# Kernel optimization log

Measured on AMD Instinct MI355X. Metric: run time of the kernel, lower is better.

The kernel has to match this reference:

```python
import jax, jax.numpy as jnp
import numpy as np

N = 100000          # n_nodes
E = 1600000         # n_edges (avg degree 16)
IN = 256            # in_dim
OUT = 16            # out_dim
SLOPE = 0.2         # leaky_relu negative slope
DROP = 0.5          # dropout rate


def _xavier(key, shape):
    fan_in, fan_out = shape
    std = (2.0 / (fan_in + fan_out)) ** 0.5
    return std * jax.random.normal(key, shape, jnp.float32)


def setup_inputs() -> dict:
    key = jax.random.key(0)
    ks = jax.random.split(key, 10)
    x = jax.random.normal(ks[0], (N, IN), jnp.float32)
    row = jax.random.randint(ks[1], (E,), 0, N, jnp.int32)
    col = jax.random.randint(ks[2], (E,), 0, N, jnp.int32)
    edge_w = jax.random.uniform(ks[3], (E,), jnp.float32)
    W1 = _xavier(ks[4], (IN, IN // 2)); b1 = jnp.zeros((IN // 2,), jnp.float32)
    W2 = _xavier(ks[5], (IN // 2, IN // 4)); b2 = jnp.zeros((IN // 4,), jnp.float32)
    W3 = _xavier(ks[6], (IN // 4, IN // 8)); b3 = jnp.zeros((IN // 8,), jnp.float32)
    W4 = _xavier(ks[7], (IN // 8, OUT)); b4 = jnp.zeros((OUT,), jnp.float32)
    # dropout mask (training-mode dropout made deterministic; pre-scaled by 1/(1-p))
    drop_mask = (jax.random.uniform(ks[8], (N, IN // 2)) > DROP).astype(jnp.float32) / (1.0 - DROP)
    return dict(x=x, row=row, col=col, edge_w=edge_w,
                W1=W1, b1=b1, W2=W2, b2=b2, W3=W3, b3=b3, W4=W4, b4=b4,
                drop_mask=drop_mask)


def reference(x, row, col, edge_w, W1, b1, W2, b2, W3, b3, W4, b4, drop_mask):
    def spmm(h):
        # out[i] = sum over edges (i <- j): w_ij * h[j]   (sparse adj @ h)
        return jax.ops.segment_sum(edge_w[:, None] * h[col], row, num_segments=N)

    lrelu = lambda v: jax.nn.leaky_relu(v, SLOPE)

    h = spmm(x @ W1) + b1          # gc1: [N, IN/2]
    h = lrelu(h) * drop_mask       # leaky_relu + dropout
    h = spmm(h @ W2) + b2          # gc2: [N, IN/4]
    h = lrelu(h)
    h = lrelu(h @ W3 + b3)         # clf hidden: [N, IN/8]
    return h @ W4 + b4             # logits: [N, OUT]
```

## Files before the change

kernel.cpp:

```cpp
#include <hip/hip_runtime.h>
#include <hip/hip_bf16.h>

#define N_NODES 100000
#define N_EDGES 1600000
#define SLOPE_ 0.2f
#define NBK 196
#define NGRP 8
#define BCAPG 1280
#define BCAP 9216
#define NCB 13
#define KEYS (512 * NCB)
#define BINBLK 256
#define PREPW 20
#define PMBLK 1563

typedef __attribute__((ext_vector_type(8))) short bf16x8;
typedef __attribute__((ext_vector_type(4))) float f32x4;

__device__ __forceinline__ short f2bf(float f) {
    __hip_bfloat16 h = __float2bfloat16(f);
    return *reinterpret_cast<short*>(&h);
}
__device__ __forceinline__ float bflo(unsigned u) { return __uint_as_float(u << 16); }
__device__ __forceinline__ float bfhi(unsigned u) { return __uint_as_float(u & 0xFFFF0000u); }
__device__ __forceinline__ float bf2f(short s) {
    return __uint_as_float(((unsigned)(unsigned short)s) << 16);
}


__global__ void zero_k(int* __restrict__ cur8) {
    for (int i = threadIdx.x; i < NBK * NGRP; i += 256) cur8[i] = 0;
}


__global__ void passA_k(const int* __restrict__ row, const int* __restrict__ col,
                        const float* __restrict__ ew, int* __restrict__ cur8,
                        int2* __restrict__ binned,
                        const float* __restrict__ W1, const float* __restrict__ W2,
                        const float* __restrict__ mask,
                        short* __restrict__ Bp1, short* __restrict__ Bp2,
                        unsigned* __restrict__ mp) {
    int t = threadIdx.x;
    if (blockIdx.x < BINBLK) {
        __shared__ int hist[NBK], base[NBK], off[NBK];
        int g = blockIdx.x & (NGRP - 1);
        const int chunk = N_EDGES / BINBLK;
        int e0 = blockIdx.x * chunk;
        for (int i = t; i < NBK; i += 256) { hist[i] = 0; off[i] = 0; }
        __syncthreads();
        for (int i = t; i < chunk; i += 256)
            atomicAdd(&hist[row[e0 + i] >> 9], 1);
        __syncthreads();
        for (int i = t; i < NBK; i += 256)
            base[i] = atomicAdd(&cur8[i * NGRP + g], hist[i]);
        __syncthreads();
        for (int i = t; i < chunk; i += 256) {
            int e = e0 + i;
            int r = row[e], c = col[e];
            int b = r >> 9;
            int p = base[b] + atomicAdd(&off[b], 1);
            if (p < BCAPG)
                binned[((size_t)(b * NGRP + g)) * BCAPG + p] =
                    make_int2(((r & 511) << 17) | c, __float_as_int(ew[e]));
        }
        return;
    }
    int bi = blockIdx.x - BINBLK;
    if (bi < PREPW) {
        int i = bi * 256 + t;
        if (i < 4096) {
            int ln = i & 15, nt = (i >> 4) & 7, g = (i >> 7) & 3, ks = i >> 9;
            int n = nt * 16 + ln, k0 = ks * 32 + g * 8;
            bf16x8 v;
#pragma unroll
            for (int j = 0; j < 8; j++) v[j] = f2bf(W1[(k0 + j) * 128 + n]);
            *(bf16x8*)(Bp1 + (size_t)i * 8) = v;
        } else if (i < 5120) {
            int c = i - 4096;
            int ln = c & 15, nt = (c >> 4) & 3, g = (c >> 6) & 3, ks = c >> 8;
            int n = nt * 16 + ln, k0 = ks * 32 + g * 8;
            bf16x8 v;
#pragma unroll
            for (int j = 0; j < 8; j++) v[j] = f2bf(W2[(k0 + j) * 64 + n]);
            *(bf16x8*)(Bp2 + (size_t)c * 8) = v;
        }
        return;
    }
    int pb = bi - PREPW;
    long fbase = (long)pb * 8192;
    int wv = t >> 6, lane = t & 63;
    const long FLIM = (long)N_NODES * 128;
    for (int it = 0; it < 32; ++it) {
        long f = fbase + it * 256 + wv * 64 + lane;
        float v = (f < FLIM) ? mask[f] : 0.f;
        unsigned long long bl = __ballot(v != 0.f);
        if (lane == 0) {
            long w = f >> 5;
            if (w < (long)N_NODES * 4)
                *(unsigned long long*)(mp + w) = bl;
        }
    }
}


__global__ void __launch_bounds__(512) passB_k(const int2* __restrict__ binned,
                                               const int* __restrict__ cur8,
                                               unsigned* __restrict__ cw,
                                               int* __restrict__ row_ptr) {
    __shared__ int hist[KEYS];
    __shared__ int offs[KEYS];
    __shared__ int ssum[512];
    __shared__ int bexc[256];
    int t = threadIdx.x, b = blockIdx.x;

    int cnt_g[NGRP];
    int cnt = 0;
#pragma unroll
    for (int g = 0; g < NGRP; g++) {
        cnt_g[g] = min(cur8[b * NGRP + g], BCAPG);
        cnt += cnt_g[g];
    }
    if (cnt > BCAP) cnt = BCAP;

    if (t < 256) {
        int tot = 0;
        if (t < NBK) {
#pragma unroll
            for (int g = 0; g < NGRP; g++) tot += min(cur8[t * NGRP + g], BCAPG);
            if (tot > BCAP) tot = BCAP;
        }
        bexc[t] = tot;
    }
    __syncthreads();
    for (int off2 = 1; off2 < 256; off2 <<= 1) {
        int v = (t < 256 && t >= off2) ? bexc[t - off2] : 0;
        __syncthreads();
        if (t < 256) bexc[t] += v;
        __syncthreads();
    }
    int gbase = bexc[b] - cnt;

    for (int i = t; i < KEYS; i += 512) hist[i] = 0;
    __syncthreads();

#pragma unroll
    for (int g = 0; g < NGRP; g++) {
        const int2* src = binned + ((size_t)(b * NGRP + g)) * BCAPG;
        int cg = cnt_g[g];
        for (int i = t; i < cg; i += 512) {
            int2 v = src[i];
            int c = v.x & 0x1FFFF, lr = v.x >> 17;
            atomicAdd(&hist[lr * NCB + (c >> 13)], 1);
        }
    }
    __syncthreads();

    int loc[NCB];
    int tot = 0;
#pragma unroll
    for (int j = 0; j < NCB; j++) {
        loc[j] = tot;
        tot += hist[t * NCB + j];
    }
    ssum[t] = tot;
    __syncthreads();
    for (int off2 = 1; off2 < 512; off2 <<= 1) {
        int v = (t >= off2) ? ssum[t - off2] : 0;
        __syncthreads();
        ssum[t] += v;
        __syncthreads();
    }
    int base = ssum[t] - tot;
#pragma unroll
    for (int j = 0; j < NCB; j++) offs[t * NCB + j] = base + loc[j];

    int grow = b * 512 + t;
    if (grow <= N_NODES) row_ptr[grow] = gbase + base;
    __syncthreads();

#pragma unroll
    for (int g = 0; g < NGRP; g++) {
        const int2* src = binned + ((size_t)(b * NGRP + g)) * BCAPG;
        int cg = cnt_g[g];
        for (int i = t; i < cg; i += 512) {
            int2 v = src[i];
            int c = v.x & 0x1FFFF, lr = v.x >> 17;
            int p = gbase + atomicAdd(&offs[lr * NCB + (c >> 13)], 1);
            unsigned wb = (unsigned)(unsigned short)f2bf(__int_as_float(v.y));
            cw[p] = ((unsigned)c << 15) | (wb & 0x7FFFu);
        }
    }
}


template <int K, int COLS, bool ABF16>
__global__ __launch_bounds__(512) void gemm_p(const void* __restrict__ Ap,
                                              const short* __restrict__ Bp,
                                              short* __restrict__ out, int M) {
    constexpr int NT = COLS / 16;
    constexpr int NKS = K / 32;
    __shared__ short Bs[K * COLS];
    int t = threadIdx.x;
    for (int i = t; i < K * COLS / 8; i += 512)
        *(bf16x8*)(Bs + (size_t)i * 8) = *(const bf16x8*)(Bp + (size_t)i * 8);
    __syncthreads();

    int l = t & 63, wv = t >> 6;
    int ln = l & 15, g = l >> 4;
    int row0 = blockIdx.x * 256 + wv * 32;
    int r0 = row0 + ln, r1 = row0 + 16 + ln;
    int cr0 = min(r0, M - 1), cr1 = min(r1, M - 1);

    f32x4 acc[2][NT];
#pragma unroll
    for (int rf = 0; rf < 2; rf++)
#pragma unroll
        for (int nt = 0; nt < NT; nt++) acc[rf][nt] = (f32x4){0.f, 0.f, 0.f, 0.f};

#pragma unroll
    for (int ks = 0; ks < NKS; ks++) {
        int kk = ks * 32 + g * 8;
        bf16x8 a0, a1;
        if constexpr (ABF16) {
            a0 = *(const bf16x8*)((const short*)Ap + (size_t)cr0 * K + kk);
            a1 = *(const bf16x8*)((const short*)Ap + (size_t)cr1 * K + kk);
        } else {
            const float* p0 = (const float*)Ap + (size_t)cr0 * K + kk;
            const float* p1 = (const float*)Ap + (size_t)cr1 * K + kk;
            float4 u0 = *(const float4*)p0;
            float4 u1 = *(const float4*)(p0 + 4);
            float4 v0 = *(const float4*)p1;
            float4 v1 = *(const float4*)(p1 + 4);
            a0[0] = f2bf(u0.x); a0[1] = f2bf(u0.y); a0[2] = f2bf(u0.z); a0[3] = f2bf(u0.w);
            a0[4] = f2bf(u1.x); a0[5] = f2bf(u1.y); a0[6] = f2bf(u1.z); a0[7] = f2bf(u1.w);
            a1[0] = f2bf(v0.x); a1[1] = f2bf(v0.y); a1[2] = f2bf(v0.z); a1[3] = f2bf(v0.w);
            a1[4] = f2bf(v1.x); a1[5] = f2bf(v1.y); a1[6] = f2bf(v1.z); a1[7] = f2bf(v1.w);
        }
#pragma unroll
        for (int nt = 0; nt < NT; nt++) {
            bf16x8 b = *(const bf16x8*)(Bs + (size_t)((((ks * 4 + g) * NT + nt) * 16 + ln)) * 8);
            acc[0][nt] = __builtin_amdgcn_mfma_f32_16x16x32_bf16(a0, b, acc[0][nt], 0, 0, 0);
            acc[1][nt] = __builtin_amdgcn_mfma_f32_16x16x32_bf16(a1, b, acc[1][nt], 0, 0, 0);
        }
    }
#pragma unroll
    for (int rf = 0; rf < 2; rf++)
#pragma unroll
        for (int nt = 0; nt < NT; nt++)
#pragma unroll
            for (int r = 0; r < 4; r++) {
                int orow = row0 + rf * 16 + g * 4 + r;
                if (orow < M) out[(size_t)orow * COLS + nt * 16 + ln] = f2bf(acc[rf][nt][r]);
            }
}


template <int D, bool DROP>
__global__ void spmm_bf(const int* __restrict__ row_ptr, const unsigned* __restrict__ cwp,
                        const short* __restrict__ h,
                        const float* __restrict__ bias, const unsigned* __restrict__ maskp,
                        short* __restrict__ out, int n) {
    int bid = blockIdx.x;
    int sbid = (bid & 7) * 3125 + (bid >> 3);
    int wid = sbid * 4 + (int)(threadIdx.x >> 6);
    int lane = threadIdx.x & 63;
    if (wid >= n) return;
    int sp = __builtin_amdgcn_readfirstlane(row_ptr[wid]);
    int ep = __builtin_amdgcn_readfirstlane(row_ptr[wid + 1]);
    int cnt = ep - sp;
    const unsigned* pcw = cwp + sp;
    const unsigned* hb = (const unsigned*)h;
    float ax = 0.f, ay = 0.f;

    if (D == 128) {
        for (int jb = 0; jb < cnt; jb += 8) {
            unsigned u[8];
            float w[8];
#pragma unroll
            for (int p = 0; p < 8; p++) {
                int idx = jb + p;
                unsigned md = pcw[idx];
                md = (idx < cnt) ? md : 0u;
                int c = (int)(md >> 15);
                w[p] = __uint_as_float((md & 0x7FFFu) << 16);
                u[p] = hb[(size_t)c * 64 + lane];
            }
#pragma unroll
            for (int p = 0; p < 8; p++) {
                ax += w[p] * bflo(u[p]);
                ay += w[p] * bfhi(u[p]);
            }
        }
        float2 b = *(const float2*)(bias + 2 * lane);
        float ox = ax + b.x, oy = ay + b.y;
        ox = ox > 0.f ? ox : SLOPE_ * ox;
        oy = oy > 0.f ? oy : SLOPE_ * oy;
        if (DROP) {
            unsigned mw = maskp[(size_t)wid * 4 + (lane >> 4)];
            unsigned sh = (2 * lane) & 31;
            ox = ((mw >> sh) & 1u) ? 2.f * ox : 0.f;
            oy = ((mw >> (sh + 1)) & 1u) ? 2.f * oy : 0.f;
        }
        unsigned ov = (unsigned)(unsigned short)f2bf(ox) |
                      ((unsigned)(unsigned short)f2bf(oy) << 16);
        *(unsigned*)(out + (size_t)wid * 128 + 2 * lane) = ov;
    } else {
        int li = lane & 31;
        for (int jb = 0; jb < cnt; jb += 8) {
            unsigned u[4];
            float w[4];
#pragma unroll
            for (int p = 0; p < 4; p++) {
                int iA = jb + 2 * p, iB = iA + 1;
                unsigned mA = pcw[iA];
                mA = (iA < cnt) ? mA : 0u;
                unsigned mB = pcw[iB];
                mB = (iB < cnt) ? mB : 0u;
                unsigned md = (lane < 32) ? mA : mB;
                int c = (int)(md >> 15);
                w[p] = __uint_as_float((md & 0x7FFFu) << 16);
                u[p] = hb[(size_t)c * 32 + li];
            }
#pragma unroll
            for (int p = 0; p < 4; p++) {
                ax += w[p] * bflo(u[p]);
                ay += w[p] * bfhi(u[p]);
            }
        }
        ax += __shfl_xor(ax, 32);
        ay += __shfl_xor(ay, 32);
        float2 b = *(const float2*)(bias + li * 2);
        float ox = ax + b.x, oy = ay + b.y;
        ox = ox > 0.f ? ox : SLOPE_ * ox;
        oy = oy > 0.f ? oy : SLOPE_ * oy;
        unsigned ov = (unsigned)(unsigned short)f2bf(ox) |
                      ((unsigned)(unsigned short)f2bf(oy) << 16);
        if (lane < 32) *(unsigned*)(out + (size_t)wid * 64 + li * 2) = ov;
    }
}


__global__ void clf_k(const short* __restrict__ h, const float* __restrict__ W3,
                      const float* __restrict__ b3, const float* __restrict__ W4,
                      const float* __restrict__ b4, float* __restrict__ out) {
    __shared__ float W3s[64][32];
    __shared__ float W4s[32][16];
    __shared__ float b3s[32], b4s[16];
    __shared__ float hs[32][64];
    __shared__ float t4[32][33];
    int t = threadIdx.x;
    for (int l = t; l < 64 * 32; l += 256) W3s[l / 32][l % 32] = W3[l];
    for (int l = t; l < 32 * 16; l += 256) W4s[l / 16][l % 16] = W4[l];
    if (t < 32) b3s[t] = b3[t];
    if (t < 16) b4s[t] = b4[t];
    int row0 = blockIdx.x * 32;
    {
        bf16x8 v = *(const bf16x8*)(h + (size_t)row0 * 64 + t * 8);
        int r = t >> 3, c0 = (t & 7) << 3;
#pragma unroll
        for (int j = 0; j < 8; j++) hs[r][c0 + j] = bf2f(v[j]);
    }
    __syncthreads();
    for (int l = t; l < 1024; l += 256) {
        int r = l / 32, c = l % 32;
        float a = b3s[c];
#pragma unroll 8
        for (int k = 0; k < 64; k++) a += hs[r][k] * W3s[k][c];
        t4[r][c] = a > 0.f ? a : SLOPE_ * a;
    }
    __syncthreads();
    for (int l = t; l < 512; l += 256) {
        int r = l / 16, c = l % 16;
        float a = b4s[c];
#pragma unroll
        for (int k = 0; k < 32; k++) a += t4[r][k] * W4s[k][c];
        out[(size_t)(row0 + r) * 16 + c] = a;
    }
}


extern "C" void kernel_launch(void* const* d_in, const int* in_sizes, int n_in,
                              void* d_out, int out_size, void* d_ws, size_t ws_size,
                              hipStream_t stream) {
    const float* x = (const float*)d_in[0];
    const int* row = (const int*)d_in[1];
    const int* col = (const int*)d_in[2];
    const float* ew = (const float*)d_in[3];
    const float* W1 = (const float*)d_in[4];
    const float* b1 = (const float*)d_in[5];
    const float* W2 = (const float*)d_in[6];
    const float* b2 = (const float*)d_in[7];
    const float* W3 = (const float*)d_in[8];
    const float* b3 = (const float*)d_in[9];
    const float* W4 = (const float*)d_in[10];
    const float* b4 = (const float*)d_in[11];
    const float* mask = (const float*)d_in[12];
    float* out = (float*)d_out;

    const int N = N_NODES, E = N_EDGES;

    short* h0 = (short*)d_ws;
    short* h1 = h0 + (size_t)N * 128;
    short* h2 = h1 + (size_t)N * 128;
    short* h3 = h2 + (size_t)N * 64;
    short* Bp1 = h3 + (size_t)N * 64;
    short* Bp2 = Bp1 + 32768;
    int* row_ptr = (int*)(Bp2 + 8192);
    int* cur8 = row_ptr + N + 1;
    unsigned* mask_p = (unsigned*)(cur8 + NBK * NGRP + 8);
    unsigned* cwp = mask_p + (size_t)N * 4;
    int2* binned = (int2*)h0;

    zero_k<<<1, 256, 0, stream>>>(cur8);
    passA_k<<<BINBLK + PREPW + PMBLK, 256, 0, stream>>>(row, col, ew, cur8, binned,
                                                        W1, W2, mask, Bp1, Bp2, mask_p);
    passB_k<<<NBK, 512, 0, stream>>>(binned, cur8, cwp, row_ptr);

    gemm_p<256, 128, false><<<(N + 255) / 256, 512, 0, stream>>>(x, Bp1, h0, N);
    spmm_bf<128, true><<<25000, 256, 0, stream>>>(row_ptr, cwp, h0, b1, mask_p, h1, N);
    gemm_p<128, 64, true><<<(N + 255) / 256, 512, 0, stream>>>(h1, Bp2, h2, N);
    spmm_bf<64, false><<<25000, 256, 0, stream>>>(row_ptr, cwp, h2, b2, nullptr, h3, N);
    clf_k<<<N / 32, 256, 0, stream>>>(h3, W3, b3, W4, b4, out);
}
```

Before: 223.7 us.

## Fuse first GEMM into binning/prep kernel with per-block W1 packing in LDS

Merges the first dense GEMM (x@W1 to bf16) into the edge-binning/mask-packing kernel. Each GEMM block now converts and packs W1 into shared memory itself, rather than reading a global Bp1 prepared earlier. The binned edge buffer moves out of h0 into its own workspace region so both can be live at once. This removes a kernel launch and lets the GEMM overlap with binning and mask packing. The cost is a large 64KB LDS allocation and 512-thread blocks for every block type, which can reduce occupancy for the binning and mask roles, and W1 is re-converted in every GEMM block.

```diff
diff --git a/kernel.cpp b/kernel.cpp
--- a/kernel.cpp
+++ b/kernel.cpp
@@ -11,8 +11,9 @@
 #define NCB 13
 #define KEYS (512 * NCB)
 #define BINBLK 256
-#define PREPW 20
+#define GEMM1B 391
 #define PMBLK 1563
+#define W2PB 4
 
 typedef __attribute__((ext_vector_type(8))) short bf16x8;
 typedef __attribute__((ext_vector_type(4))) float f32x4;
@@ -33,28 +34,32 @@
 }
 
 
-__global__ void passA_k(const int* __restrict__ row, const int* __restrict__ col,
-                        const float* __restrict__ ew, int* __restrict__ cur8,
-                        int2* __restrict__ binned,
-                        const float* __restrict__ W1, const float* __restrict__ W2,
-                        const float* __restrict__ mask,
-                        short* __restrict__ Bp1, short* __restrict__ Bp2,
-                        unsigned* __restrict__ mp) {
+__global__ __launch_bounds__(512) void mega_k(
+        const int* __restrict__ row, const int* __restrict__ col,
+        const float* __restrict__ ew, int* __restrict__ cur8,
+        int2* __restrict__ binned,
+        const float* __restrict__ x, const float* __restrict__ W1,
+        const float* __restrict__ W2, const float* __restrict__ mask,
+        short* __restrict__ h0, short* __restrict__ Bp2,
+        unsigned* __restrict__ mp, int M) {
+    __shared__ int hist[NBK], base[NBK], off[NBK];
+    __shared__ short Bs[32768];
     int t = threadIdx.x;
-    if (blockIdx.x < BINBLK) {
-        __shared__ int hist[NBK], base[NBK], off[NBK];
-        int g = blockIdx.x & (NGRP - 1);
+    unsigned bx = blockIdx.x;
+
+    if (bx < BINBLK) {
+        int g = bx & (NGRP - 1);
         const int chunk = N_EDGES / BINBLK;
-        int e0 = blockIdx.x * chunk;
-        for (int i = t; i < NBK; i += 256) { hist[i] = 0; off[i] = 0; }
-        __syncthreads();
-        for (int i = t; i < chunk; i += 256)
+        int e0 = bx * chunk;
+        for (int i = t; i < NBK; i += 512) { hist[i] = 0; off[i] = 0; }
+        __syncthreads();
+        for (int i = t; i < chunk; i += 512)
             atomicAdd(&hist[row[e0 + i] >> 9], 1);
         __syncthreads();
-        for (int i = t; i < NBK; i += 256)
+        for (int i = t; i < NBK; i += 512)
             base[i] = atomicAdd(&cur8[i * NGRP + g], hist[i]);
         __syncthreads();
-        for (int i = t; i < chunk; i += 256) {
+        for (int i = t; i < chunk; i += 512) {
             int e = e0 + i;
             int r = row[e], c = col[e];
             int b = r >> 9;
@@ -65,40 +70,87 @@
         }
         return;
     }
-    int bi = blockIdx.x - BINBLK;
-    if (bi < PREPW) {
-        int i = bi * 256 + t;
-        if (i < 4096) {
-            int ln = i & 15, nt = (i >> 4) & 7, g = (i >> 7) & 3, ks = i >> 9;
-            int n = nt * 16 + ln, k0 = ks * 32 + g * 8;
+    if (bx < BINBLK + GEMM1B) {
+        constexpr int K = 256, NT = 8, NKS = K / 32;
+        for (int i = t; i < 4096; i += 512) {
+            int ln = i & 15, nt = (i >> 4) & 7, gg = (i >> 7) & 3, ks = i >> 9;
+            int n = nt * 16 + ln, k0 = ks * 32 + gg * 8;
             bf16x8 v;
 #pragma unroll
             for (int j = 0; j < 8; j++) v[j] = f2bf(W1[(k0 + j) * 128 + n]);
-            *(bf16x8*)(Bp1 + (size_t)i * 8) = v;
-        } else if (i < 5120) {
-            int c = i - 4096;
-            int ln = c & 15, nt = (c >> 4) & 3, g = (c >> 6) & 3, ks = c >> 8;
-            int n = nt * 16 + ln, k0 = ks * 32 + g * 8;
-            bf16x8 v;
-#pragma unroll
-            for (int j = 0; j < 8; j++) v[j] = f2bf(W2[(k0 + j) * 64 + n]);
-            *(bf16x8*)(Bp2 + (size_t)c * 8) = v;
-        }
+            *(bf16x8*)(Bs + (size_t)i * 8) = v;
+        }
+        __syncthreads();
+
+        int l = t & 63, wv = t >> 6;
+        int ln = l & 15, g = l >> 4;
+        int row0 = (bx - BINBLK) * 256 + wv * 32;
+        int r0 = row0 + ln, r1 = row0 + 16 + ln;
+        int cr0 = min(r0, M - 1), cr1 = min(r1, M - 1);
+
+        f32x4 acc[2][NT];
+#pragma unroll
+        for (int rf = 0; rf < 2; rf++)
+#pragma unroll
+            for (int nt = 0; nt < NT; nt++) acc[rf][nt] = (f32x4){0.f, 0.f, 0.f, 0.f};
+
+#pragma unroll
+        for (int ks = 0; ks < NKS; ks++) {
+            int kk = ks * 32 + g * 8;
+            const float* p0 = x + (size_t)cr0 * K + kk;
+            const float* p1 = x + (size_t)cr1 * K + kk;
+            float4 u0 = *(const float4*)p0;
+            float4 u1 = *(const float4*)(p0 + 4);
+            float4 v0 = *(const float4*)p1;
+            float4 v1 = *(const float4*)(p1 + 4);
+            bf16x8 a0, a1;
+            a0[0] = f2bf(u0.x); a0[1] = f2bf(u0.y); a0[2] = f2bf(u0.z); a0[3] = f2bf(u0.w);
+            a0[4] = f2bf(u1.x); a0[5] = f2bf(u1.y); a0[6] = f2bf(u1.z); a0[7] = f2bf(u1.w);
+            a1[0] = f2bf(v0.x); a1[1] = f2bf(v0.y); a1[2] = f2bf(v0.z); a1[3] = f2bf(v0.w);
+            a1[4] = f2bf(v1.x); a1[5] = f2bf(v1.y); a1[6] = f2bf(v1.z); a1[7] = f2bf(v1.w);
+#pragma unroll
+            for (int nt = 0; nt < NT; nt++) {
+                bf16x8 b = *(const bf16x8*)(Bs + (size_t)((((ks * 4 + g) * NT + nt) * 16 + ln)) * 8);
+                acc[0][nt] = __builtin_amdgcn_mfma_f32_16x16x32_bf16(a0, b, acc[0][nt], 0, 0, 0);
+                acc[1][nt] = __builtin_amdgcn_mfma_f32_16x16x32_bf16(a1, b, acc[1][nt], 0, 0, 0);
+            }
+        }
+#pragma unroll
+        for (int rf = 0; rf < 2; rf++)
+#pragma unroll
+            for (int nt = 0; nt < NT; nt++)
+#pragma unroll
+                for (int r = 0; r < 4; r++) {
+                    int orow = row0 + rf * 16 + g * 4 + r;
+                    if (orow < M) h0[(size_t)orow * 128 + nt * 16 + ln] = f2bf(acc[rf][nt][r]);
+                }
         return;
     }
-    int pb = bi - PREPW;
-    long fbase = (long)pb * 8192;
-    int wv = t >> 6, lane = t & 63;
-    const long FLIM = (long)N_NODES * 128;
-    for (int it = 0; it < 32; ++it) {
-        long f = fbase + it * 256 + wv * 64 + lane;
-        float v = (f < FLIM) ? mask[f] : 0.f;
-        unsigned long long bl = __ballot(v != 0.f);
-        if (lane == 0) {
-            long w = f >> 5;
-            if (w < (long)N_NODES * 4)
-                *(unsigned long long*)(mp + w) = bl;
-        }
+    if (bx < BINBLK + GEMM1B + PMBLK) {
+        int pb = bx - (BINBLK + GEMM1B);
+        long fbase = (long)pb * 8192;
+        int lane = t & 63;
+        const long FLIM = (long)N_NODES * 128;
+        for (int it = 0; it < 16; ++it) {
+            long f = fbase + it * 512 + t;
+            float v = (f < FLIM) ? mask[f] : 0.f;
+            unsigned long long bl = __ballot(v != 0.f);
+            if (lane == 0) {
+                long w = f >> 5;
+                if (w < (long)N_NODES * 4)
+                    *(unsigned long long*)(mp + w) = bl;
+            }
+        }
+        return;
+    }
+    int c = (bx - (BINBLK + GEMM1B + PMBLK)) * 512 + t;
+    if (c < 1024) {
+        int ln = c & 15, nt = (c >> 4) & 3, gg = (c >> 6) & 3, ks = c >> 8;
+        int n = nt * 16 + ln, k0 = ks * 32 + gg * 8;
+        bf16x8 v;
+#pragma unroll
+        for (int j = 0; j < 8; j++) v[j] = f2bf(W2[(k0 + j) * 64 + n]);
+        *(bf16x8*)(Bp2 + (size_t)c * 8) = v;
     }
 }
 
@@ -403,20 +455,18 @@
     short* h1 = h0 + (size_t)N * 128;
     short* h2 = h1 + (size_t)N * 128;
     short* h3 = h2 + (size_t)N * 64;
-    short* Bp1 = h3 + (size_t)N * 64;
-    short* Bp2 = Bp1 + 32768;
+    short* Bp2 = h3 + (size_t)N * 64;
     int* row_ptr = (int*)(Bp2 + 8192);
     int* cur8 = row_ptr + N + 1;
     unsigned* mask_p = (unsigned*)(cur8 + NBK * NGRP + 8);
     unsigned* cwp = mask_p + (size_t)N * 4;
-    int2* binned = (int2*)h0;
+    int2* binned = (int2*)(cwp + E + 16);
 
     zero_k<<<1, 256, 0, stream>>>(cur8);
-    passA_k<<<BINBLK + PREPW + PMBLK, 256, 0, stream>>>(row, col, ew, cur8, binned,
-                                                        W1, W2, mask, Bp1, Bp2, mask_p);
+    mega_k<<<BINBLK + GEMM1B + PMBLK + W2PB, 512, 0, stream>>>(
+        row, col, ew, cur8, binned, x, W1, W2, mask, h0, Bp2, mask_p, N);
     passB_k<<<NBK, 512, 0, stream>>>(binned, cur8, cwp, row_ptr);
 
-    gemm_p<256, 128, false><<<(N + 255) / 256, 512, 0, stream>>>(x, Bp1, h0, N);
     spmm_bf<128, true><<<25000, 256, 0, stream>>>(row_ptr, cwp, h0, b1, mask_p, h1, N);
     gemm_p<128, 64, true><<<(N + 255) / 256, 512, 0, stream>>>(h1, Bp2, h2, N);
     spmm_bf<64, false><<<25000, 256, 0, stream>>>(row_ptr, cwp, h2, b2, nullptr, h3, N);
```

Result: slower. 233.8 us (+4.5%).

## Store first GEMM output in column slices and slice the first SpMM

Applied to the files above, without the earlier changes.

The first GEMM now writes its output as 8 column slices of 16 features each, laid out [slice][node][16]. A new SpMM kernel has each block handle one slice for 32 rows, so the gathered feature table per slice (about 3.2MB) is more likely to stay resident in cache during the random gathers. Each wave processes 8 edges at a time with 8 lanes per edge, then reduces across lanes with shuffles. The trade-off is that the edge list is read 8 times, and each row now uses a short, lane-underutilised reduction with serial per-row iteration.

```diff
diff --git a/kernel.cpp b/kernel.cpp
--- a/kernel.cpp
+++ b/kernel.cpp
@@ -26,6 +26,7 @@
 __device__ __forceinline__ float bf2f(short s) {
     return __uint_as_float(((unsigned)(unsigned short)s) << 16);
 }
+__device__ __forceinline__ float lrelu_(float v) { return v > 0.f ? v : SLOPE_ * v; }
 
 
 __global__ void zero_k(int* __restrict__ cur8) {
@@ -193,7 +194,7 @@
 }
 
 
-template <int K, int COLS, bool ABF16>
+template <int K, int COLS, bool ABF16, bool SLICE>
 __global__ __launch_bounds__(512) void gemm_p(const void* __restrict__ Ap,
                                               const short* __restrict__ Bp,
                                               short* __restrict__ out, int M) {
@@ -250,16 +251,66 @@
 #pragma unroll
             for (int r = 0; r < 4; r++) {
                 int orow = row0 + rf * 16 + g * 4 + r;
-                if (orow < M) out[(size_t)orow * COLS + nt * 16 + ln] = f2bf(acc[rf][nt][r]);
+                if (orow < M) {
+                    if constexpr (SLICE)
+                        out[((size_t)nt * M + orow) * 16 + ln] = f2bf(acc[rf][nt][r]);
+                    else
+                        out[(size_t)orow * COLS + nt * 16 + ln] = f2bf(acc[rf][nt][r]);
+                }
             }
 }
 
 
-template <int D, bool DROP>
-__global__ void spmm_bf(const int* __restrict__ row_ptr, const unsigned* __restrict__ cwp,
+__global__ void spmm_sl(const int* __restrict__ row_ptr, const unsigned* __restrict__ cwp,
+                        const unsigned* __restrict__ h0s,
+                        const float* __restrict__ b1, const unsigned* __restrict__ maskp,
+                        short* __restrict__ out, int n) {
+    int bid = blockIdx.x;
+    int s = bid & 7;
+    int rg = bid >> 3;
+    int wv = threadIdx.x >> 6;
+    int lane = threadIdx.x & 63;
+    int eg = lane >> 3, wd = lane & 7;
+    int row0 = rg * 32 + wv * 8;
+    const unsigned* hs = h0s + (size_t)s * n * 8;
+
+    for (int ri = 0; ri < 8; ri++) {
+        int r = row0 + ri;
+        int sp = __builtin_amdgcn_readfirstlane(row_ptr[r]);
+        int ep = __builtin_amdgcn_readfirstlane(row_ptr[r + 1]);
+        int cnt = ep - sp;
+        const unsigned* pcw = cwp + sp;
+        float ax = 0.f, ay = 0.f;
+        for (int jb = 0; jb < cnt; jb += 8) {
+            int idx = jb + eg;
+            unsigned md = __builtin_nontemporal_load(pcw + idx);
+            md = (idx < cnt) ? md : 0u;
+            int c = (int)(md >> 15);
+            float w = __uint_as_float((md & 0x7FFFu) << 16);
+            unsigned u = hs[(size_t)c * 8 + wd];
+            ax += w * bflo(u);
+            ay += w * bfhi(u);
+        }
+        ax += __shfl_xor(ax, 8); ax += __shfl_xor(ax, 16); ax += __shfl_xor(ax, 32);
+        ay += __shfl_xor(ay, 8); ay += __shfl_xor(ay, 16); ay += __shfl_xor(ay, 32);
+        if (lane < 8) {
+            int d0 = s * 16 + 2 * lane;
+            float ox = lrelu_(ax + b1[d0]), oy = lrelu_(ay + b1[d0 + 1]);
+            unsigned mw = maskp[(size_t)r * 4 + (d0 >> 5)];
+            int sh = d0 & 31;
+            ox = ((mw >> sh) & 1u) ? 2.f * ox : 0.f;
+            oy = ((mw >> (sh + 1)) & 1u) ? 2.f * oy : 0.f;
+            unsigned ov = (unsigned)(unsigned short)f2bf(ox) |
+                          ((unsigned)(unsigned short)f2bf(oy) << 16);
+            __builtin_nontemporal_store(ov, (unsigned*)out + (size_t)r * 64 + s * 8 + lane);
+        }
+    }
+}
+
+
+__global__ void spmm2_k(const int* __restrict__ row_ptr, const unsigned* __restrict__ cwp,
                         const short* __restrict__ h,
-                        const float* __restrict__ bias, const unsigned* __restrict__ maskp,
-                        short* __restrict__ out, int n) {
+                        const float* __restrict__ bias, short* __restrict__ out, int n) {
     int bid = blockIdx.x;
     int sbid = (bid & 7) * 3125 + (bid >> 3);
     int wid = sbid * 4 + (int)(threadIdx.x >> 6);
@@ -270,73 +321,36 @@
     int cnt = ep - sp;
     const unsigned* pcw = cwp + sp;
     const unsigned* hb = (const unsigned*)h;
+    int li = lane & 31;
     float ax = 0.f, ay = 0.f;
-
-    if (D == 128) {
-        for (int jb = 0; jb < cnt; jb += 8) {
-            unsigned u[8];
-            float w[8];
-#pragma unroll
-            for (int p = 0; p < 8; p++) {
-                int idx = jb + p;
-                unsigned md = pcw[idx];
-                md = (idx < cnt) ? md : 0u;
-                int c = (int)(md >> 15);
-                w[p] = __uint_as_float((md & 0x7FFFu) << 16);
-                u[p] = hb[(size_t)c * 64 + lane];
-            }
-#pragma unroll
-            for (int p = 0; p < 8; p++) {
-                ax += w[p] * bflo(u[p]);
-                ay += w[p] * bfhi(u[p]);
-            }
-        }
-        float2 b = *(const float2*)(bias + 2 * lane);
-        float ox = ax + b.x, oy = ay + b.y;
-        ox = ox > 0.f ? ox : SLOPE_ * ox;
-        oy = oy > 0.f ? oy : SLOPE_ * oy;
-        if (DROP) {
-            unsigned mw = maskp[(size_t)wid * 4 + (lane >> 4)];
-            unsigned sh = (2 * lane) & 31;
-            ox = ((mw >> sh) & 1u) ? 2.f * ox : 0.f;
-            oy = ((mw >> (sh + 1)) & 1u) ? 2.f * oy : 0.f;
-        }
-        unsigned ov = (unsigned)(unsigned short)f2bf(ox) |
-                      ((unsigned)(unsigned short)f2bf(oy) << 16);
-        *(unsigned*)(out + (size_t)wid * 128 + 2 * lane) = ov;
-    } else {
-        int li = lane & 31;
-        for (int jb = 0; jb < cnt; jb += 8) {
-            unsigned u[4];
-            float w[4];
-#pragma unroll
-            for (int p = 0; p < 4; p++) {
-                int iA = jb + 2 * p, iB = iA + 1;
-                unsigned mA = pcw[iA];
-                mA = (iA < cnt) ? mA : 0u;
-                unsigned mB = pcw[iB];
-                mB = (iB < cnt) ? mB : 0u;
-                unsigned md = (lane < 32) ? mA : mB;
-                int c = (int)(md >> 15);
-                w[p] = __uint_as_float((md & 0x7FFFu) << 16);
-                u[p] = hb[(size_t)c * 32 + li];
-            }
-#pragma unroll
-            for (int p = 0; p < 4; p++) {
-                ax += w[p] * bflo(u[p]);
-                ay += w[p] * bfhi(u[p]);
-            }
-        }
-        ax += __shfl_xor(ax, 32);
-        ay += __shfl_xor(ay, 32);
-        float2 b = *(const float2*)(bias + li * 2);
-        float ox = ax + b.x, oy = ay + b.y;
-        ox = ox > 0.f ? ox : SLOPE_ * ox;
-        oy = oy > 0.f ? oy : SLOPE_ * oy;
-        unsigned ov = (unsigned)(unsigned short)f2bf(ox) |
-                      ((unsigned)(unsigned short)f2bf(oy) << 16);
-        if (lane < 32) *(unsigned*)(out + (size_t)wid * 64 + li * 2) = ov;
-    }
+    for (int jb = 0; jb < cnt; jb += 8) {
+        unsigned u[4];
+        float w[4];
+#pragma unroll
+        for (int p = 0; p < 4; p++) {
+            int iA = jb + 2 * p, iB = iA + 1;
+            unsigned mA = pcw[iA];
+            mA = (iA < cnt) ? mA : 0u;
+            unsigned mB = pcw[iB];
+            mB = (iB < cnt) ? mB : 0u;
+            unsigned md = (lane < 32) ? mA : mB;
+            int c = (int)(md >> 15);
+            w[p] = __uint_as_float((md & 0x7FFFu) << 16);
+            u[p] = hb[(size_t)c * 32 + li];
+        }
+#pragma unroll
+        for (int p = 0; p < 4; p++) {
+            ax += w[p] * bflo(u[p]);
+            ay += w[p] * bfhi(u[p]);
+        }
+    }
+    ax += __shfl_xor(ax, 32);
+    ay += __shfl_xor(ay, 32);
+    float2 b = *(const float2*)(bias + li * 2);
+    float ox = lrelu_(ax + b.x), oy = lrelu_(ay + b.y);
+    unsigned ov = (unsigned)(unsigned short)f2bf(ox) |
+                  ((unsigned)(unsigned short)f2bf(oy) << 16);
+    if (lane < 32) *(unsigned*)(out + (size_t)wid * 64 + li * 2) = ov;
 }
 
 
@@ -416,9 +430,9 @@
                                                         W1, W2, mask, Bp1, Bp2, mask_p);
     passB_k<<<NBK, 512, 0, stream>>>(binned, cur8, cwp, row_ptr);
 
-    gemm_p<256, 128, false><<<(N + 255) / 256, 512, 0, stream>>>(x, Bp1, h0, N);
-    spmm_bf<128, true><<<25000, 256, 0, stream>>>(row_ptr, cwp, h0, b1, mask_p, h1, N);
-    gemm_p<128, 64, true><<<(N + 255) / 256, 512, 0, stream>>>(h1, Bp2, h2, N);
-    spmm_bf<64, false><<<25000, 256, 0, stream>>>(row_ptr, cwp, h2, b2, nullptr, h3, N);
+    gemm_p<256, 128, false, true><<<(N + 255) / 256, 512, 0, stream>>>(x, Bp1, h0, N);
+    spmm_sl<<<25000, 256, 0, stream>>>(row_ptr, cwp, (const unsigned*)h0, b1, mask_p, h1, N);
+    gemm_p<128, 64, true, false><<<(N + 255) / 256, 512, 0, stream>>>(h1, Bp2, h2, N);
+    spmm2_k<<<25000, 256, 0, stream>>>(row_ptr, cwp, h2, b2, h3, N);
     clf_k<<<N / 32, 256, 0, stream>>>(h3, W3, b3, W4, b4, out);
 }
```

After: 476.8 us. +113.2%, slower.
